# Kernel optimization log

Measured on AMD Instinct MI355X. Metric: run time of the kernel, lower is better.

The kernel has to match this reference:

```python
import jax, jax.numpy as jnp
import numpy as np

N = 100000        # nodes
E = 3200000       # edges (before self-loops)
F_IN = 16         # data.num_features
H = 2             # heads (both layers)
C1, C2 = 8, 4     # per-head out channels of conv1 / conv2
NEG_SLOPE = 0.2   # PyG GATConv default


def setup_inputs() -> dict:
    key = jax.random.key(0)
    ks = jax.random.split(key, 10)
    x = jax.random.normal(ks[0], (N, F_IN), jnp.float32)
    edge_index = jax.random.randint(ks[1], (2, E), 0, N)  # [src; dst]

    def glorot(k, shape):
        fan = shape[0] + shape[-1]
        return jax.random.normal(k, shape, jnp.float32) * jnp.sqrt(2.0 / fan)

    # conv1: 16 -> 8, heads=2 (concat -> 16)
    W1 = glorot(ks[2], (F_IN, H * C1))
    att_src1 = glorot(ks[3], (H, C1))
    att_dst1 = glorot(ks[4], (H, C1))
    b1 = jnp.zeros((H * C1,), jnp.float32)
    # conv2: 16 -> 4, heads=2 (concat -> 8)
    W2 = glorot(ks[5], (H * C1, H * C2))
    att_src2 = glorot(ks[6], (H, C2))
    att_dst2 = glorot(ks[7], (H, C2))
    b2 = jnp.zeros((H * C2,), jnp.float32)
    return {"x": x, "edge_index": edge_index,
            "W1": W1, "att_src1": att_src1, "att_dst1": att_dst1, "b1": b1,
            "W2": W2, "att_src2": att_src2, "att_dst2": att_dst2, "b2": b2}


def gat_conv(x, src, dst, W, a_src, a_dst, b):
    """PyG-style GATConv: gather + edge logits + per-dst segment softmax + scatter."""
    n = x.shape[0]
    h_heads, c = a_src.shape
    h = (x @ W).reshape(n, h_heads, c)                       # [N,H,C]
    al_s = jnp.einsum('nhc,hc->nh', h, a_src)                # [N,H]
    al_d = jnp.einsum('nhc,hc->nh', h, a_dst)                # [N,H]
    e = jax.nn.leaky_relu(al_s[src] + al_d[dst], NEG_SLOPE)  # [E,H]
    m = jax.ops.segment_max(e, dst, num_segments=n)          # per-dst max
    m = jnp.where(jnp.isfinite(m), m, 0.0)
    w = jnp.exp(e - m[dst])
    z = jax.ops.segment_sum(w, dst, num_segments=n)
    alpha = w / (z[dst] + 1e-16)                             # [E,H]
    out = jax.ops.segment_sum(alpha[:, :, None] * h[src], dst, num_segments=n)
    return out.reshape(n, h_heads * c) + b


def reference(x, edge_index, W1, att_src1, att_dst1, b1, W2, att_src2, att_dst2, b2):
    n = x.shape[0]
    loop = jnp.arange(n, dtype=edge_index.dtype)             # add_self_loops=True
    src = jnp.concatenate([edge_index[0], loop])
    dst = jnp.concatenate([edge_index[1], loop])
    h = gat_conv(x, src, dst, W1, att_src1, att_dst1, b1)
    h = jax.nn.elu(h)
    # dropout(p=0.6, training=self.training) -> identity in eval mode
    return gat_conv(h, src, dst, W2, att_src2, att_dst2, b2)
```

## Files before the change

kernel.cpp:

```cpp
#include <hip/hip_runtime.h>
#include <hip/hip_bf16.h>

#define TB 256
#define TBB 1024
#define BSH 8
#define BSZ 256
#define CHUNK 8192
#define CAP 9216
#define TLS 1024

__device__ __forceinline__ float ldany(const void* __restrict__ p, size_t i, int isf32) {
  if (isf32) return ((const float*)p)[i];
  unsigned int u = ((const unsigned short*)p)[i];
  return __uint_as_float(u << 16);
}

__device__ __forceinline__ unsigned f2bf2(float lo, float hi) {
  unsigned ul = __float_as_uint(lo), uh = __float_as_uint(hi);
  ul += 0x7FFFu + ((ul >> 16) & 1u);
  uh += 0x7FFFu + ((uh >> 16) & 1u);
  return (ul >> 16) | (uh & 0xFFFF0000u);
}
__device__ __forceinline__ unsigned short f2bf1(float x) {
  unsigned u = __float_as_uint(x);
  u += 0x7FFFu + ((u >> 16) & 1u);
  return (unsigned short)(u >> 16);
}
__device__ __forceinline__ float bf_lo(unsigned u) { return __uint_as_float(u << 16); }
__device__ __forceinline__ float bf_hi(unsigned u) { return __uint_as_float(u & 0xFFFF0000u); }

__device__ __forceinline__ int detect_isf(const unsigned short* __restrict__ xb) {
  int lane = threadIdx.x & 63;
  int mx = 0;
  #pragma unroll
  for (int j = 0; j < 4; ++j) { int e = (xb[lane * 4 + j] >> 7) & 0xFF; mx = max(mx, e); }
  #pragma unroll
  for (int off = 32; off > 0; off >>= 1) mx = max(mx, __shfl_xor(mx, off));
  return mx > 160;
}

__global__ __launch_bounds__(TBB) void
k_scatter_proj(const int* __restrict__ ei, int E, int Et, int NB, int EB,
               int* __restrict__ gcur, int* __restrict__ packed,
               const unsigned short* __restrict__ xb,
               const void* __restrict__ Wg, const void* __restrict__ adg,
               unsigned* __restrict__ hb, float* __restrict__ ald, int n) {
  __shared__ int shmem[512];
  if (blockIdx.x < EB) {
    int* lcnt = shmem;
    for (int i = threadIdx.x; i < NB; i += TBB) lcnt[i] = 0;
    __syncthreads();
    long b0 = (long)blockIdx.x * CHUNK;
    int cnt = (int)(((long)Et - b0 < (long)CHUNK) ? ((long)Et - b0) : (long)CHUNK);
    for (int i = threadIdx.x * 4; i < cnt; i += TBB * 4) {
      long e = b0 + i;
      int rem = cnt - i;
      if (rem >= 4 && e + 3 < (long)E) {
        int4 d4 = *(const int4*)(ei + E + e);
        atomicAdd(&lcnt[d4.x >> BSH], 1);
        atomicAdd(&lcnt[d4.y >> BSH], 1);
        atomicAdd(&lcnt[d4.z >> BSH], 1);
        atomicAdd(&lcnt[d4.w >> BSH], 1);
      } else {
        int m = rem < 4 ? rem : 4;
        for (int j = 0; j < m; ++j) {
          long ee = e + j;
          int d = (ee < E) ? ei[E + ee] : (int)(ee - E);
          atomicAdd(&lcnt[d >> BSH], 1);
        }
      }
    }
    __syncthreads();
    if (threadIdx.x < NB) {
      int c = lcnt[threadIdx.x];
      lcnt[threadIdx.x] = threadIdx.x * CAP + (c ? atomicAdd(&gcur[threadIdx.x], c) : 0);
    }
    __syncthreads();
    for (int i = threadIdx.x * 4; i < cnt; i += TBB * 4) {
      long e = b0 + i;
      int rem = cnt - i;
      if (rem >= 4 && e + 3 < (long)E) {
        int4 s4 = *(const int4*)(ei + e);
        int4 d4 = *(const int4*)(ei + E + e);
        int bk, pos;
        bk = d4.x >> BSH; pos = atomicAdd(&lcnt[bk], 1); packed[pos] = ((d4.x & (BSZ-1)) << 17) | s4.x;
        bk = d4.y >> BSH; pos = atomicAdd(&lcnt[bk], 1); packed[pos] = ((d4.y & (BSZ-1)) << 17) | s4.y;
        bk = d4.z >> BSH; pos = atomicAdd(&lcnt[bk], 1); packed[pos] = ((d4.z & (BSZ-1)) << 17) | s4.z;
        bk = d4.w >> BSH; pos = atomicAdd(&lcnt[bk], 1); packed[pos] = ((d4.w & (BSZ-1)) << 17) | s4.w;
      } else {
        int m = rem < 4 ? rem : 4;
        for (int j = 0; j < m; ++j) {
          long ee = e + j;
          int s, d;
          if (ee < E) { s = ei[ee]; d = ei[E + ee]; }
          else        { s = (int)(ee - E); d = s; }
          int bk = d >> BSH;
          int pos = atomicAdd(&lcnt[bk], 1);
          packed[pos] = ((d & (BSZ - 1)) << 17) | s;
        }
      }
    }
  } else {
    const int isf = detect_isf(xb);
    float* Ws = (float*)shmem;
    __shared__ float ad_s[16];
    for (int i = threadIdx.x; i < 256; i += TBB) Ws[i] = ldany(Wg, i, isf);
    if (threadIdx.x < 16) ad_s[threadIdx.x] = ldany(adg, threadIdx.x, isf);
    __syncthreads();
    int nid = (blockIdx.x - EB) * TBB + threadIdx.x;
    if (nid >= n) return;

    float xr[16];
    #pragma unroll
    for (int i = 0; i < 16; ++i) xr[i] = ldany(xb, (size_t)nid * 16 + i, isf);

    float hv[16];
    #pragma unroll
    for (int j = 0; j < 16; ++j) hv[j] = 0.f;
    #pragma unroll
    for (int k = 0; k < 16; ++k) {
      #pragma unroll
      for (int j = 0; j < 16; ++j) hv[j] += xr[k] * Ws[k * 16 + j];
    }

    unsigned* row = hb + (size_t)nid * 8;
    ((uint4*)row)[0] = make_uint4(f2bf2(hv[0], hv[1]),  f2bf2(hv[2], hv[3]),
                                  f2bf2(hv[4], hv[5]),  f2bf2(hv[6], hv[7]));
    ((uint4*)row)[1] = make_uint4(f2bf2(hv[8], hv[9]),  f2bf2(hv[10], hv[11]),
                                  f2bf2(hv[12], hv[13]), f2bf2(hv[14], hv[15]));

    float d0 = 0.f, d1 = 0.f;
    #pragma unroll
    for (int c = 0; c < 8; ++c) {
      d0 += hv[c] * ad_s[c];
      d1 += hv[8 + c] * ad_s[8 + c];
    }
    ((float2*)ald)[nid] = make_float2(d0, d1);
  }
}

__global__ __launch_bounds__(TLS) void k_localsort(const int* __restrict__ gcur,
                                                   const int* __restrict__ packed,
                                                   int* __restrict__ rowptr,
                                                   int* __restrict__ csr,
                                                   int n) {
  __shared__ int lcnt[BSZ], lbase[BSZ], sh[BSZ];
  const int b = blockIdx.x;
  const int node0 = b << BSH;
  const int tid = threadIdx.x;
  const int beg = b * CAP;
  const int end = beg + gcur[b];
  if (tid < BSZ) lcnt[tid] = 0;
  __syncthreads();
  for (int k = beg + tid; k < end; k += TLS)
    atomicAdd(&lcnt[packed[k] >> 17], 1);
  __syncthreads();
  int v = (tid < BSZ) ? lcnt[tid] : 0;
  if (tid < BSZ) sh[tid] = v;
  __syncthreads();
  for (int off = 1; off < BSZ; off <<= 1) {
    int t = (tid < BSZ && tid >= off) ? sh[tid - off] : 0;
    __syncthreads();
    if (tid < BSZ) sh[tid] += t;
    __syncthreads();
  }
  if (tid < BSZ) lbase[tid] = sh[tid] - v;
  __syncthreads();
  const int nn = min(BSZ, n - node0);
  if (tid < nn) rowptr[b * (BSZ + 1) + tid] = beg + lbase[tid];
  if (tid == 0) rowptr[b * (BSZ + 1) + nn] = end;
  for (int k = beg + tid; k < end; k += TLS) {
    int p = packed[k];
    int dl = p >> 17;
    int pos = beg + atomicAdd(&lbase[dl], 1);
    csr[pos] = p & 0x1FFFF;
  }
}

__global__ __launch_bounds__(TB) void
gat_gather1(const int* __restrict__ rowptr, const int* __restrict__ csr,
            const unsigned* __restrict__ hb, const float* __restrict__ ald,
            const void* __restrict__ bias, const void* __restrict__ as1g,
            const void* __restrict__ W2g, const void* __restrict__ ad2g,
            unsigned* __restrict__ hb2, float* __restrict__ ald2,
            int n, const unsigned short* __restrict__ xb) {
  const int isf = detect_isf(xb);
  __shared__ float sb[16];
  __shared__ float as1s[16];
  __shared__ float W2s[128];
  __shared__ float ad2s[8];
  if (threadIdx.x < 16) sb[threadIdx.x] = ldany(bias, threadIdx.x, isf);
  if (threadIdx.x >= 16 && threadIdx.x < 32) as1s[threadIdx.x - 16] = ldany(as1g, threadIdx.x - 16, isf);
  if (threadIdx.x >= 32 && threadIdx.x < 40) ad2s[threadIdx.x - 32] = ldany(ad2g, threadIdx.x - 32, isf);
  if (threadIdx.x >= 128) W2s[threadIdx.x - 128] = ldany(W2g, threadIdx.x - 128, isf);
  __syncthreads();

  const int t = blockIdx.x * TB + threadIdx.x;
  const int sub = t & 15, nid = t >> 4;
  const int slot = sub >> 1, hq = sub & 1;
  const bool act = nid < n;
  int beg = 0, end = 0;
  float aldv = 0.f;
  float as_r[8];
  #pragma unroll
  for (int c = 0; c < 8; ++c) as_r[c] = as1s[hq * 8 + c];
  if (act) {
    int g = nid + (nid >> BSH);
    beg = rowptr[g];
    end = rowptr[g + 1];
    aldv = ald[(size_t)nid * 2 + hq];
  }

  float acc[8];
  #pragma unroll
  for (int c = 0; c < 8; ++c) acc[c] = 0.f;
  float z = 0.f;

  int k  = beg + slot;
  int kn = k + 8;
  int s_cur = (k  < end) ? csr[k]  : 0;
  int s_nxt = (kn < end) ? csr[kn] : 0;
  uint4 u_cur = *(const uint4*)(hb + (size_t)s_cur * 8 + hq * 4);
  while (k < end) {
    uint4 u_n = *(const uint4*)(hb + (size_t)s_nxt * 8 + hq * 4);
    int kf = kn + 8;
    int s_f = (kf < end) ? csr[kf] : 0;
    float h0 = bf_lo(u_cur.x), h1 = bf_hi(u_cur.x);
    float h2 = bf_lo(u_cur.y), h3 = bf_hi(u_cur.y);
    float h4 = bf_lo(u_cur.z), h5 = bf_hi(u_cur.z);
    float h6 = bf_lo(u_cur.w), h7 = bf_hi(u_cur.w);
    float alsv = h0 * as_r[0] + h1 * as_r[1] + h2 * as_r[2] + h3 * as_r[3]
               + h4 * as_r[4] + h5 * as_r[5] + h6 * as_r[6] + h7 * as_r[7];
    float lg = alsv + aldv;
    lg = lg > 0.f ? lg : 0.2f * lg;
    float w = __expf(lg);
    z += w;
    acc[0] += w * h0; acc[1] += w * h1; acc[2] += w * h2; acc[3] += w * h3;
    acc[4] += w * h4; acc[5] += w * h5; acc[6] += w * h6; acc[7] += w * h7;
    k = kn; kn = kf; s_cur = s_nxt; s_nxt = s_f; u_cur = u_n;
  }

  #pragma unroll
  for (int off = 2; off < 16; off <<= 1) {
    z += __shfl_xor(z, off);
    #pragma unroll
    for (int c = 0; c < 8; ++c) acc[c] += __shfl_xor(acc[c], off);
  }
  float inv = 1.f / (z + 1e-16f);

  float v_[8];
  #pragma unroll
  for (int c = 0; c < 8; ++c) {
    float v = acc[c] * inv + sb[hq * 8 + c];
    v_[c] = v > 0.f ? v : expm1f(v);
  }

  const int lg = (threadIdx.x & 63) & ~15;
  const int out = sub & 7;
  float h2v = 0.f;
  #pragma unroll
  for (int kk = 0; kk < 16; ++kk) {
    float vk = __shfl(v_[kk & 7], lg + (kk >> 3));
    h2v += vk * W2s[kk * 8 + out];
  }
  if (act && sub < 8)
    ((unsigned short*)hb2)[(size_t)nid * 8 + out] = f2bf1(h2v);

  float part = h2v * ad2s[out];
  part += __shfl_xor(part, 1);
  part += __shfl_xor(part, 2);
  float d21 = __shfl(part, lg + 4);
  if (act && sub == 0)
    ((float2*)ald2)[nid] = make_float2(part, d21);
}

__global__ __launch_bounds__(TB) void
gat_gather2(const int* __restrict__ rowptr, const int* __restrict__ csr,
            const unsigned* __restrict__ hb2, const float* __restrict__ ald2,
            const void* __restrict__ bias, const void* __restrict__ as2g,
            void* __restrict__ outp, int n, const unsigned short* __restrict__ xb) {
  const int isf = detect_isf(xb);
  __shared__ float sb[8];
  __shared__ float as2s[8];
  if (threadIdx.x < 8) sb[threadIdx.x] = ldany(bias, threadIdx.x, isf);
  if (threadIdx.x >= 8 && threadIdx.x < 16) as2s[threadIdx.x - 8] = ldany(as2g, threadIdx.x - 8, isf);
  __syncthreads();

  const int t = blockIdx.x * TB + threadIdx.x;
  const int sub = t & 15, nid = t >> 4;
  const int slot = sub >> 1, hq = sub & 1;
  const bool act = nid < n;
  int beg = 0, end = 0;
  float aldv = 0.f;
  float as_r[4];
  #pragma unroll
  for (int c = 0; c < 4; ++c) as_r[c] = as2s[hq * 4 + c];
  if (act) {
    int g = nid + (nid >> BSH);
    beg = rowptr[g];
    end = rowptr[g + 1];
    aldv = ald2[(size_t)nid * 2 + hq];
  }

  float a0 = 0.f, a1 = 0.f, a2 = 0.f, a3 = 0.f, z = 0.f;

  int k  = beg + slot;
  int kn = k + 8;
  int s_cur = (k  < end) ? csr[k]  : 0;
  int s_nxt = (kn < end) ? csr[kn] : 0;
  uint2 u_cur = *(const uint2*)(hb2 + (size_t)s_cur * 4 + hq * 2);
  while (k < end) {
    uint2 u_n = *(const uint2*)(hb2 + (size_t)s_nxt * 4 + hq * 2);
    int kf = kn + 8;
    int s_f = (kf < end) ? csr[kf] : 0;
    float h0 = bf_lo(u_cur.x), h1 = bf_hi(u_cur.x);
    float h2 = bf_lo(u_cur.y), h3 = bf_hi(u_cur.y);
    float alsv = h0 * as_r[0] + h1 * as_r[1] + h2 * as_r[2] + h3 * as_r[3];
    float lg = alsv + aldv;
    lg = lg > 0.f ? lg : 0.2f * lg;
    float w = __expf(lg);
    z += w;
    a0 += w * h0; a1 += w * h1; a2 += w * h2; a3 += w * h3;
    k = kn; kn = kf; s_cur = s_nxt; s_nxt = s_f; u_cur = u_n;
  }

  #pragma unroll
  for (int off = 2; off < 16; off <<= 1) {
    z  += __shfl_xor(z, off);
    a0 += __shfl_xor(a0, off); a1 += __shfl_xor(a1, off);
    a2 += __shfl_xor(a2, off); a3 += __shfl_xor(a3, off);
  }

  if (act && slot == 0) {
    float inv = 1.f / (z + 1e-16f);
    float v0 = a0 * inv + sb[hq * 4 + 0];
    float v1 = a1 * inv + sb[hq * 4 + 1];
    float v2 = a2 * inv + sb[hq * 4 + 2];
    float v3 = a3 * inv + sb[hq * 4 + 3];
    if (isf) {
      ((float4*)outp)[(size_t)nid * 2 + hq] = make_float4(v0, v1, v2, v3);
    } else {
      ((uint2*)outp)[(size_t)nid * 2 + hq] = make_uint2(f2bf2(v0, v1), f2bf2(v2, v3));
    }
  }
}

extern "C" void kernel_launch(void* const* d_in, const int* in_sizes, int n_in,
                              void* d_out, int out_size, void* d_ws, size_t ws_size,
                              hipStream_t stream) {
  const unsigned short* xb = (const unsigned short*)d_in[0];
  const int*  ei  = (const int*)d_in[1];
  const void* W1  = d_in[2];
  const void* as1 = d_in[3];
  const void* ad1 = d_in[4];
  const void* b1  = d_in[5];
  const void* W2  = d_in[6];
  const void* as2 = d_in[7];
  const void* ad2 = d_in[8];
  const void* b2  = d_in[9];

  const int n  = in_sizes[0] / 16;
  const int E  = in_sizes[1] / 2;
  const int Et = E + n;
  const int NB = (n + BSZ - 1) >> BSH;
  const int EB = (Et + CHUNK - 1) / CHUNK;

  char* base = (char*)d_ws;
  int* gcur   = (int*)(base + 64);
  int* rowptr = gcur + NB;
  int* packed = rowptr + NB * (BSZ + 1);
  int* csr    = packed + (size_t)NB * CAP;
  size_t off1 = 64 + sizeof(int) * ((size_t)NB + (size_t)NB * (BSZ + 1)
                                    + 2 * (size_t)NB * CAP);
  off1 = (off1 + 255) & ~(size_t)255;
  unsigned* hb1  = (unsigned*)(base + off1);
  float*    ald1 = (float*)(base + off1 + (size_t)32 * n);
  size_t off2 = off1 + (size_t)40 * n;
  off2 = (off2 + 255) & ~(size_t)255;
  unsigned* hb2  = (unsigned*)(base + off2);
  float*    ald2 = (float*)(base + off2 + (size_t)16 * n);

  const int pblk = (n + TBB - 1) / TBB;
  const int gblk = (16 * n + TB - 1) / TB;

  hipMemsetAsync(gcur, 0, (size_t)NB * sizeof(int), stream);
  k_scatter_proj<<<EB + pblk, TBB, 0, stream>>>(ei, E, Et, NB, EB, gcur, packed,
                                                xb, W1, ad1, hb1, ald1, n);
  k_localsort<<<NB, TLS, 0, stream>>>(gcur, packed, rowptr, csr, n);

  gat_gather1<<<gblk, TB, 0, stream>>>(rowptr, csr, hb1, ald1, b1, as1,
                                       W2, ad2, hb2, ald2, n, xb);

  gat_gather2<<<gblk, TB, 0, stream>>>(rowptr, csr, hb2, ald2, b2, as2,
                                       d_out, n, xb);
}
```

Before: 119.2 us.

## Halve scatter chunk to one int4 per thread; share 16B row loads across head lanes

The edge-bucketing phase now uses a chunk of 4096 edges so each thread handles exactly one int4 of edges. Each thread keeps its edges in registers between the count pass and the scatter pass, so the edge list is not read from memory a second time. In the layer-2 gather, only the even lane loads the full 16-byte hidden row and the odd (second-head) lane gets its half through shuffles. This replaces two 8-byte loads with one 16-byte load. In exchange the scatter launches twice as many blocks with more global cursor atomics, and the gather adds shuffle traffic and a divergent load inside its loop.

```diff
diff --git a/kernel.cpp b/kernel.cpp
--- a/kernel.cpp
+++ b/kernel.cpp
@@ -5,7 +5,7 @@
 #define TBB 1024
 #define BSH 8
 #define BSZ 256
-#define CHUNK 8192
+#define CHUNK 4096
 #define CAP 9216
 #define TLS 1024
 
@@ -50,56 +50,43 @@
     int* lcnt = shmem;
     for (int i = threadIdx.x; i < NB; i += TBB) lcnt[i] = 0;
     __syncthreads();
-    long b0 = (long)blockIdx.x * CHUNK;
-    int cnt = (int)(((long)Et - b0 < (long)CHUNK) ? ((long)Et - b0) : (long)CHUNK);
-    for (int i = threadIdx.x * 4; i < cnt; i += TBB * 4) {
-      long e = b0 + i;
-      int rem = cnt - i;
-      if (rem >= 4 && e + 3 < (long)E) {
-        int4 d4 = *(const int4*)(ei + E + e);
-        atomicAdd(&lcnt[d4.x >> BSH], 1);
-        atomicAdd(&lcnt[d4.y >> BSH], 1);
-        atomicAdd(&lcnt[d4.z >> BSH], 1);
-        atomicAdd(&lcnt[d4.w >> BSH], 1);
+    long e = (long)blockIdx.x * CHUNK + threadIdx.x * 4;
+    int4 s4 = make_int4(0, 0, 0, 0), d4 = make_int4(0, 0, 0, 0);
+    int m = 0;
+    if (e < Et) {
+      long rem = Et - e;
+      m = rem < 4 ? (int)rem : 4;
+      if (m == 4 && e + 3 < (long)E) {
+        s4 = *(const int4*)(ei + e);
+        d4 = *(const int4*)(ei + E + e);
       } else {
-        int m = rem < 4 ? rem : 4;
+        int ss[4], dd[4];
         for (int j = 0; j < m; ++j) {
           long ee = e + j;
-          int d = (ee < E) ? ei[E + ee] : (int)(ee - E);
-          atomicAdd(&lcnt[d >> BSH], 1);
+          if (ee < E) { ss[j] = ei[ee]; dd[j] = ei[E + ee]; }
+          else        { ss[j] = (int)(ee - E); dd[j] = ss[j]; }
         }
+        s4.x = ss[0]; d4.x = dd[0];
+        if (m > 1) { s4.y = ss[1]; d4.y = dd[1]; }
+        if (m > 2) { s4.z = ss[2]; d4.z = dd[2]; }
+        if (m > 3) { s4.w = ss[3]; d4.w = dd[3]; }
       }
     }
+    if (m > 0) atomicAdd(&lcnt[d4.x >> BSH], 1);
+    if (m > 1) atomicAdd(&lcnt[d4.y >> BSH], 1);
+    if (m > 2) atomicAdd(&lcnt[d4.z >> BSH], 1);
+    if (m > 3) atomicAdd(&lcnt[d4.w >> BSH], 1);
     __syncthreads();
     if (threadIdx.x < NB) {
       int c = lcnt[threadIdx.x];
       lcnt[threadIdx.x] = threadIdx.x * CAP + (c ? atomicAdd(&gcur[threadIdx.x], c) : 0);
     }
     __syncthreads();
-    for (int i = threadIdx.x * 4; i < cnt; i += TBB * 4) {
-      long e = b0 + i;
-      int rem = cnt - i;
-      if (rem >= 4 && e + 3 < (long)E) {
-        int4 s4 = *(const int4*)(ei + e);
-        int4 d4 = *(const int4*)(ei + E + e);
-        int bk, pos;
-        bk = d4.x >> BSH; pos = atomicAdd(&lcnt[bk], 1); packed[pos] = ((d4.x & (BSZ-1)) << 17) | s4.x;
-        bk = d4.y >> BSH; pos = atomicAdd(&lcnt[bk], 1); packed[pos] = ((d4.y & (BSZ-1)) << 17) | s4.y;
-        bk = d4.z >> BSH; pos = atomicAdd(&lcnt[bk], 1); packed[pos] = ((d4.z & (BSZ-1)) << 17) | s4.z;
-        bk = d4.w >> BSH; pos = atomicAdd(&lcnt[bk], 1); packed[pos] = ((d4.w & (BSZ-1)) << 17) | s4.w;
-      } else {
-        int m = rem < 4 ? rem : 4;
-        for (int j = 0; j < m; ++j) {
-          long ee = e + j;
-          int s, d;
-          if (ee < E) { s = ei[ee]; d = ei[E + ee]; }
-          else        { s = (int)(ee - E); d = s; }
-          int bk = d >> BSH;
-          int pos = atomicAdd(&lcnt[bk], 1);
-          packed[pos] = ((d & (BSZ - 1)) << 17) | s;
-        }
-      }
-    }
+    int bk, pos;
+    if (m > 0) { bk = d4.x >> BSH; pos = atomicAdd(&lcnt[bk], 1); packed[pos] = ((d4.x & (BSZ-1)) << 17) | s4.x; }
+    if (m > 1) { bk = d4.y >> BSH; pos = atomicAdd(&lcnt[bk], 1); packed[pos] = ((d4.y & (BSZ-1)) << 17) | s4.y; }
+    if (m > 2) { bk = d4.z >> BSH; pos = atomicAdd(&lcnt[bk], 1); packed[pos] = ((d4.z & (BSZ-1)) << 17) | s4.z; }
+    if (m > 3) { bk = d4.w >> BSH; pos = atomicAdd(&lcnt[bk], 1); packed[pos] = ((d4.w & (BSZ-1)) << 17) | s4.w; }
   } else {
     const int isf = detect_isf(xb);
     float* Ws = (float*)shmem;
@@ -289,6 +276,7 @@
   const int t = blockIdx.x * TB + threadIdx.x;
   const int sub = t & 15, nid = t >> 4;
   const int slot = sub >> 1, hq = sub & 1;
+  const int even = (threadIdx.x & 63) & ~1;
   const bool act = nid < n;
   int beg = 0, end = 0;
   float aldv = 0.f;
@@ -308,13 +296,18 @@
   int kn = k + 8;
   int s_cur = (k  < end) ? csr[k]  : 0;
   int s_nxt = (kn < end) ? csr[kn] : 0;
-  uint2 u_cur = *(const uint2*)(hb2 + (size_t)s_cur * 4 + hq * 2);
+  uint4 u_cur = make_uint4(0, 0, 0, 0);
+  if (hq == 0) u_cur = *(const uint4*)(hb2 + (size_t)s_cur * 4);
   while (k < end) {
-    uint2 u_n = *(const uint2*)(hb2 + (size_t)s_nxt * 4 + hq * 2);
+    uint4 u_n = make_uint4(0, 0, 0, 0);
+    if (hq == 0) u_n = *(const uint4*)(hb2 + (size_t)s_nxt * 4);
     int kf = kn + 8;
     int s_f = (kf < end) ? csr[kf] : 0;
-    float h0 = bf_lo(u_cur.x), h1 = bf_hi(u_cur.x);
-    float h2 = bf_lo(u_cur.y), h3 = bf_hi(u_cur.y);
+    unsigned q0 = __shfl(u_cur.x, even), q1 = __shfl(u_cur.y, even);
+    unsigned q2 = __shfl(u_cur.z, even), q3 = __shfl(u_cur.w, even);
+    unsigned m0 = hq ? q2 : q0, m1 = hq ? q3 : q1;
+    float h0 = bf_lo(m0), h1 = bf_hi(m0);
+    float h2 = bf_lo(m1), h3 = bf_hi(m1);
     float alsv = h0 * as_r[0] + h1 * as_r[1] + h2 * as_r[2] + h3 * as_r[3];
     float lg = alsv + aldv;
     lg = lg > 0.f ? lg : 0.2f * lg;
```

Result: slower. 132.3 us (+11.1%).
